# Kernel optimization log

Measured on AMD Instinct MI355X. Metric: run time of the kernel, lower is better.

## Reference

```python
import jax, jax.numpy as jnp
import numpy as np

IMG = 128
HW = IMG // 2          # render resolution (img_size // 2)
NPTS = 64              # samples per ray
MIN_D, MAX_D = 1.2, 2.8
VOL_PHYS = 1.0         # physical volume size; voxel = VOL_PHYS / D
B, C, D = 8, 16, 64
EPS_EA = 1e-10         # pytorch3d EmissionAbsorption eps
BN_EPS = 1e-5


def setup_inputs():
    key = jax.random.key(0)
    ks = jax.random.split(key, 6)
    R = jnp.tile(jnp.eye(3, dtype=jnp.float32)[None], (B, 1, 1))
    T = jnp.tile(jnp.array([0.0, 0.0, 2.0], jnp.float32)[None], (B, 1))
    K = jnp.tile(jnp.array([[180.0, 0.0, 64.0], [0.0, 180.0, 64.0], [0.0, 0.0, 1.0]],
                           jnp.float32)[None], (B, 1, 1))
    feature_3d = jax.random.normal(ks[0], (B, C, D, D, D), jnp.float32)
    density_3d = jax.random.uniform(ks[1], (B, 1, D, D, D), jnp.float32)
    wt = jax.random.normal(ks[2], (16, 16, 6, 6), jnp.float32) * 0.05
    bt = jnp.zeros((16,), jnp.float32)
    g1 = jnp.ones((16,), jnp.float32); be1 = jnp.zeros((16,), jnp.float32)
    w1 = jax.random.normal(ks[3], (8, 16, 5, 5), jnp.float32) * 0.05
    b1 = jnp.zeros((8,), jnp.float32)
    g2 = jnp.ones((8,), jnp.float32); be2 = jnp.zeros((8,), jnp.float32)
    w2 = jax.random.normal(ks[4], (3, 8, 5, 5), jnp.float32) * 0.05
    b2 = jnp.zeros((3,), jnp.float32)
    return dict(R=R, T=T, K=K, feature_3d=feature_3d, density_3d=density_3d,
                wt=wt, bt=bt, g1=g1, be1=be1, w1=w1, b1=b1, g2=g2, be2=be2,
                w2=w2, b2=b2)


def _trilerp(vol, pts):
    # vol [C,Dz,Dy,Dx]; pts [N,3] xyz in [-1,1]; grid_sample align_corners=True, zero padding
    Cc, Dz, Dy, Dx = vol.shape
    ix = (pts[:, 0] + 1.0) * 0.5 * (Dx - 1)
    iy = (pts[:, 1] + 1.0) * 0.5 * (Dy - 1)
    iz = (pts[:, 2] + 1.0) * 0.5 * (Dz - 1)
    x0f = jnp.floor(ix); y0f = jnp.floor(iy); z0f = jnp.floor(iz)
    fx, fy, fz = ix - x0f, iy - y0f, iz - z0f
    x0 = x0f.astype(jnp.int32); y0 = y0f.astype(jnp.int32); z0 = z0f.astype(jnp.int32)
    out = jnp.zeros((Cc, pts.shape[0]), vol.dtype)
    for dz in (0, 1):
        for dy in (0, 1):
            for dx in (0, 1):
                xc, yc, zc = x0 + dx, y0 + dy, z0 + dz
                w = ((fx if dx else 1.0 - fx) * (fy if dy else 1.0 - fy)
                     * (fz if dz else 1.0 - fz))
                valid = ((xc >= 0) & (xc < Dx) & (yc >= 0) & (yc < Dy)
                         & (zc >= 0) & (zc < Dz))
                v = vol[:, jnp.clip(zc, 0, Dz - 1), jnp.clip(yc, 0, Dy - 1),
                        jnp.clip(xc, 0, Dx - 1)]
                out = out + (w * valid) * v
    return out  # [C,N]


def _bn(x, g, b):
    m = x.mean((0, 2, 3), keepdims=True)
    v = x.var((0, 2, 3), keepdims=True)
    return g[None, :, None, None] * (x - m) * jax.lax.rsqrt(v + BN_EPS) + b[None, :, None, None]


def _leaky(x):
    return jnp.where(x >= 0, x, 0.01 * x)


def _conv(x, w, b, pad):
    y = jax.lax.conv_general_dilated(x, w, (1, 1), [(pad, pad), (pad, pad)],
                                     dimension_numbers=('NCHW', 'OIHW', 'NCHW'))
    return y + b[None, :, None, None]


def _conv_t(x, w, b):
    # torch ConvTranspose2d(k=6, stride=2, pad=2) == dilated conv with flipped, io-swapped kernel
    wf = jnp.flip(w, (-2, -1)).transpose(1, 0, 2, 3)
    y = jax.lax.conv_general_dilated(x, wf, (1, 1), [(3, 3), (3, 3)],
                                     lhs_dilation=(2, 2),
                                     dimension_numbers=('NCHW', 'OIHW', 'NCHW'))
    return y + b[None, :, None, None]


def _forward(R, T, K, feature_3d, density_3d, wt, bt, g1, be1, w1, b1, g2, be2, w2, b2):
    Bb, Cc, Dv, Hv, Wv = feature_3d.shape
    # K /= 2; K[:,-1,-1] = 1 (non-mutating)
    Kh = (K / 2.0).at[:, 2, 2].set(1.0)
    fx, fy = Kh[:, 0, 0], Kh[:, 1, 1]
    cx, cy = Kh[:, 0, 2], Kh[:, 1, 2]
    # pixel-center grid at half resolution (NDCGridRaysampler pixel centers)
    u = jnp.arange(HW, dtype=jnp.float32) + 0.5
    v = jnp.arange(HW, dtype=jnp.float32) + 0.5
    ddx = (u[None, None, :] - cx[:, None, None]) / fx[:, None, None]  # [B,1,W]
    ddy = (v[None, :, None] - cy[:, None, None]) / fy[:, None, None]  # [B,H,1]
    one = jnp.ones((1, 1, 1), jnp.float32)
    dirs_cam = jnp.stack(jnp.broadcast_arrays(ddx, ddy, one), axis=-1)  # [B,H,W,3]
    dirs_w = jnp.einsum('bji,bhwj->bhwi', R, dirs_cam)                  # R^T d
    origin = -jnp.einsum('bji,bj->bi', R, T)                            # cam center
    depths = jnp.linspace(MIN_D, MAX_D, NPTS, dtype=jnp.float32)
    pts = (origin[:, None, None, None, :]
           + dirs_w[:, :, :, None, :] * depths[None, None, None, :, None])  # [B,H,W,P,3]
    # world -> Volumes local coords (align_corners=True span: voxel*(dim-1))
    voxel = VOL_PHYS / Dv
    scale = jnp.array([2.0 / (voxel * (Wv - 1)), 2.0 / (voxel * (Hv - 1)),
                       2.0 / (voxel * (Dv - 1))], jnp.float32)
    loc = (pts * scale).reshape(Bb, -1, 3)
    vol = jnp.concatenate([feature_3d, density_3d], axis=1)  # [B,C+1,D,H,W]
    samp = jax.vmap(_trilerp)(vol, loc)                      # [B,C+1,N]
    samp = samp.reshape(Bb, Cc + 1, HW, HW, NPTS)
    feats = jnp.moveaxis(samp[:, :Cc], 1, -1)                # [B,H,W,P,C]
    sigma = samp[:, Cc]                                      # [B,H,W,P]
    # EmissionAbsorption raymarcher (shifted cumprod, shift=1)
    cp = jnp.cumprod((1.0 + EPS_EA) - sigma, axis=-1)
    absorb = jnp.concatenate([jnp.ones_like(cp[..., :1]), cp[..., :-1]], axis=-1)
    wgt = sigma * absorb
    img = jnp.einsum('bhwp,bhwpc->bhwc', wgt, feats)
    opac = 1.0 - jnp.prod(1.0 - sigma, axis=-1)
    imgs = jnp.moveaxis(img, -1, 1)        # [B,C,HW,HW]
    sil = opac[:, None]                    # [B,1,HW,HW]
    # conv refine head
    x = _conv_t(imgs, wt, bt)              # [B,16,128,128]
    x = _leaky(_bn(x, g1, be1))
    x = _conv(x, w1, b1, pad=2)
    x = _leaky(_bn(x, g2, be2))
    x = _conv(x, w2, b2, pad=2)
    imgs_out = jax.nn.relu(x)
    sil_up = jax.image.resize(sil, (Bb, 1, IMG, IMG), 'bilinear')
    return imgs_out, sil_up


def reference(R, T, K, feature_3d, density_3d, wt, bt, g1, be1, w1, b1, g2, be2, w2, b2):
    return _forward(R, T, K, feature_3d, density_3d, wt, bt, g1, be1, w1, b1,
                    g2, be2, w2, b2)
```

## Files before the change

### kernel.cpp

```cpp
#include <hip/hip_runtime.h>
#include <hip/hip_bf16.h>

typedef __hip_bfloat16 bf16;
typedef unsigned int uint;
typedef unsigned short ushort;

using frag  = __attribute__((ext_vector_type(8))) short;
using f32x4 = __attribute__((ext_vector_type(4))) float;

__device__ bf16  g_volT[8ULL*262144*16];
__device__ bf16  g_imgT[8*4096*16];
__device__ bf16  g_t1 [8*16384*16];
__device__ bf16  g_a2r[8*16384*8];
__device__ float g_sil[8*4096];
__device__ float g_part [512*32];
__device__ float g_part2[256*16];
__device__ float g_stats[96];
__device__ bf16  g_wAt[4*5*64*8];
__device__ bf16  g_wA1[13*64*8];
__device__ bf16  g_wA2[7*64*8];

__device__ __forceinline__ float bup(ushort u){ union{uint u; float f;} x; x.u = ((uint)u)<<16; return x.f; }
__device__ __forceinline__ ushort bdn(float f){ union{ bf16 h; ushort s;} v; v.h = __float2bfloat16(f); return v.s; }
__device__ __forceinline__ uint aff2(uint u, float a0, float b0, float a1, float b1){
  float x0 = bup((ushort)(u & 0xffff)), x1 = bup((ushort)(u >> 16));
  float y0 = fmaf(a0, x0, b0); y0 = y0 >= 0.f ? y0 : 0.01f*y0;
  float y1 = fmaf(a1, x1, b1); y1 = y1 >= 0.f ? y1 : 0.01f*y1;
  return (uint)bdn(y0) | ((uint)bdn(y1) << 16);
}
__device__ __forceinline__ f32x4 mf(frag a, frag b, f32x4 c){
  return __builtin_amdgcn_mfma_f32_16x16x32_bf16(a, b, c, 0, 0, 0);
}
__device__ __forceinline__ void acc2(uint u, float w, float& a, float& b){
  union { uint u; float f; } lo, hi;
  lo.u = u << 16; hi.u = u & 0xffff0000u;
  a = fmaf(w, lo.f, a); b = fmaf(w, hi.f, b);
}

__global__ __launch_bounds__(256) void k_wprep(const float* __restrict__ wt,
                                               const float* __restrict__ w1,
                                               const float* __restrict__ w2)
{
  int tid = threadIdx.x;
  for (int idx = tid; idx < 4*5*64*8; idx += 256){
    int cls = idx / 2560; int rem = idx % 2560;
    int step = rem / 512; int rem2 = rem % 512;
    int lane = rem2 >> 3, j = rem2 & 7;
    int o = lane & 15;
    int k = step*32 + (lane>>4)*8 + j;
    int tau = k >> 4, ic = k & 15;
    int dr = cls >> 1, dc = cls & 1;
    float val = 0.f;
    if (tau < 9){
      int s = tau/3, t = tau%3;
      val = wt[(ic*16 + o)*36 + (4-2*s+dr)*6 + (4-2*t+dc)];
    }
    g_wAt[idx] = __float2bfloat16(val);
  }
  for (int idx = tid; idx < 13*64*8; idx += 256){
    int step = idx / 512; int rem2 = idx % 512;
    int lane = rem2 >> 3, j = rem2 & 7;
    int o = lane & 15;
    int k = step*32 + (lane>>4)*8 + j;
    int tau = k >> 4, ic = k & 15;
    float val = (tau < 25 && o < 8) ? w1[o*400 + ic*25 + tau] : 0.f;
    g_wA1[idx] = __float2bfloat16(val);
  }
  for (int idx = tid; idx < 7*64*8; idx += 256){
    int step = idx / 512; int rem2 = idx % 512;
    int lane = rem2 >> 3, j = rem2 & 7;
    int o = lane & 15;
    int k = step*32 + (lane>>4)*8 + j;
    int tau = k >> 3, ic = k & 7;
    float val = (tau < 25 && o < 3) ? w2[o*200 + ic*25 + tau] : 0.f;
    g_wA2[idx] = __float2bfloat16(val);
  }
}

__global__ __launch_bounds__(256) void k_transpose(const float* __restrict__ feat)
{
  __shared__ float lt[64*17];
  int blk = blockIdx.x;
  int y = blk & 63, z = (blk>>6)&63, b = blk>>12;
  const float* src = feat + (size_t)b*16*262144 + z*4096 + y*64;
  #pragma unroll
  for (int it=0; it<4; ++it){
    int idx = it*256 + threadIdx.x;
    int c = idx>>6, x = idx&63;
    lt[x*17+c] = src[(size_t)c*262144 + x];
  }
  __syncthreads();
  uint* dst = (uint*)(g_volT + (size_t)blk*1024);
  #pragma unroll
  for (int it=0; it<2; ++it){
    int idx = it*256 + threadIdx.x;
    int x = idx>>3, c2 = (idx&7)*2;
    uint lo = bdn(lt[x*17+c2]);
    uint hi = bdn(lt[x*17+c2+1]);
    dst[idx] = lo | (hi<<16);
  }
}

__global__ __launch_bounds__(256) void k_render(
    const float* __restrict__ R, const float* __restrict__ T, const float* __restrict__ Kin,
    const float* __restrict__ dens)
{
  __shared__ float lds_acc[4][64][17];
  __shared__ float lds_T[4][64];
  __shared__ float lds_P[4][64];

  int blk  = blockIdx.x;
  int tid  = threadIdx.x;
  int wv   = tid >> 6;
  int lane = tid & 63;
  int b  = blk & 7;
  int t  = blk >> 3;
  int py0 = (t >> 3) * 8, px0 = (t & 7) * 8;
  int h = py0 + (lane >> 3), w = px0 + (lane & 7);

  float fx = Kin[b*9+0]*0.5f, fy = Kin[b*9+4]*0.5f;
  float cx = Kin[b*9+2]*0.5f, cy = Kin[b*9+5]*0.5f;
  float u = (float)w + 0.5f, v = (float)h + 0.5f;
  float dcx = (u - cx)/fx, dcy = (v - cy)/fy;
  float Rm[9];
  #pragma unroll
  for (int i=0;i<9;i++) Rm[i] = R[b*9+i];
  float T0 = T[b*3+0], T1 = T[b*3+1], T2 = T[b*3+2];
  float dwx = Rm[0]*dcx + Rm[3]*dcy + Rm[6];
  float dwy = Rm[1]*dcx + Rm[4]*dcy + Rm[7];
  float dwz = Rm[2]*dcx + Rm[5]*dcy + Rm[8];
  float ox = -(Rm[0]*T0 + Rm[3]*T1 + Rm[6]*T2);
  float oy = -(Rm[1]*T0 + Rm[4]*T1 + Rm[7]*T2);
  float oz = -(Rm[2]*T0 + Rm[5]*T1 + Rm[8]*T2);

  const float SC = 2.0f*64.0f/63.0f;
  const float* dp = dens + (size_t)b*262144;
  const bf16* vb = g_volT + (size_t)b*262144*16;

  float vch[16];
  #pragma unroll
  for (int c=0;c<16;c++) vch[c] = 0.f;
  float Trun = 1.0f, Pop = 1.0f;

  for (int i=0;i<16;i++){
    float depth = 1.2f + (1.6f/63.0f) * (float)(wv*16 + i);
    float ix = (ox + dwx*depth)*SC;  ix = (ix + 1.0f)*0.5f*63.0f;
    float iy = (oy + dwy*depth)*SC;  iy = (iy + 1.0f)*0.5f*63.0f;
    float iz = (oz + dwz*depth)*SC;  iz = (iz + 1.0f)*0.5f*63.0f;
    float xf = floorf(ix), yf = floorf(iy), zf = floorf(iz);
    float fxr = ix-xf, fyr = iy-yf, fzr = iz-zf;
    int x0 = (int)xf, y0 = (int)yf, z0 = (int)zf;

    int offs[8]; float cw[8];
    #pragma unroll
    for (int k=0;k<8;k++){
      int dx = k&1, dy=(k>>1)&1, dz=(k>>2)&1;
      int xc=x0+dx, yc=y0+dy, zc=z0+dz;
      bool valid = (xc>=0)&(xc<64)&(yc>=0)&(yc<64)&(zc>=0)&(zc<64);
      float wk = (dx?fxr:1.f-fxr)*(dy?fyr:1.f-fyr)*(dz?fzr:1.f-fzr);
      cw[k] = valid ? wk : 0.0f;
      int xcc = min(max(xc,0),63), ycc=min(max(yc,0),63), zcc=min(max(zc,0),63);
      offs[k] = (zcc*64 + ycc)*64 + xcc;
    }
    float sigma = 0.f;
    #pragma unroll
    for (int k=0;k<8;k++) sigma += cw[k]*dp[offs[k]];

    float wgt = sigma * Trun;
    Trun *= (1.0f + 1e-10f - sigma);
    Pop  *= (1.0f - sigma);

    #pragma unroll
    for (int k=0;k<8;k++){
      const uint4* p = (const uint4*)(vb + (size_t)offs[k]*16);
      uint4 q0 = p[0];
      uint4 q1 = p[1];
      float wk = cw[k]*wgt;
      acc2(q0.x, wk, vch[0],  vch[1]);
      acc2(q0.y, wk, vch[2],  vch[3]);
      acc2(q0.z, wk, vch[4],  vch[5]);
      acc2(q0.w, wk, vch[6],  vch[7]);
      acc2(q1.x, wk, vch[8],  vch[9]);
      acc2(q1.y, wk, vch[10], vch[11]);
      acc2(q1.z, wk, vch[12], vch[13]);
      acc2(q1.w, wk, vch[14], vch[15]);
    }
  }

  #pragma unroll
  for (int c=0;c<16;c++) lds_acc[wv][lane][c] = vch[c];
  lds_T[wv][lane] = Trun;
  lds_P[wv][lane] = Pop;
  __syncthreads();

  {
    int p  = wv*16 + (lane >> 2);
    int c0 = (lane & 3) * 4;
    float pref = 1.0f;
    float s0=0.f, s1=0.f, s2=0.f, s3=0.f;
    #pragma unroll
    for (int ww=0; ww<4; ++ww){
      s0 += pref * lds_acc[ww][p][c0+0];
      s1 += pref * lds_acc[ww][p][c0+1];
      s2 += pref * lds_acc[ww][p][c0+2];
      s3 += pref * lds_acc[ww][p][c0+3];
      pref *= lds_T[ww][p];
    }
    int hh = py0 + (p >> 3), ww2 = px0 + (p & 7);
    if ((lane & 3) == 0){
      float P = lds_P[0][p]*lds_P[1][p]*lds_P[2][p]*lds_P[3][p];
      g_sil[b*4096 + hh*64 + ww2] = 1.0f - P;
    }
    uint lo = (uint)bdn(s0) | ((uint)bdn(s1) << 16);
    uint hi = (uint)bdn(s2) | ((uint)bdn(s3) << 16);
    uint2 pk; pk.x = lo; pk.y = hi;
    *(uint2*)(g_imgT + ((size_t)(b*4096) + hh*64 + ww2)*16 + c0) = pk;
  }
}

__global__ __launch_bounds__(256) void k_convt(const float* __restrict__ bt)
{
  __shared__ __align__(16) short tile[3*66*16];
  __shared__ float ssum[4][16], ssq[4][16];

  int blk = blockIdx.x;
  int r = blk & 63, b = blk >> 6;
  int tid = threadIdx.x;

  for (int idx = tid; idx < 396; idx += 256){
    int row3 = idx / 132; int rem = idx - row3*132;
    int c2 = rem >> 1, half = rem & 1;
    int gr = r - 1 + row3, gc = c2 - 1;
    uint4 val = make_uint4(0,0,0,0);
    if (gr>=0 && gr<64 && gc>=0 && gc<64)
      val = *(const uint4*)(g_imgT + ((size_t)(b*4096) + gr*64 + gc)*16 + half*8);
    *(uint4*)(tile + (row3*66 + c2)*16 + half*8) = val;
  }
  __syncthreads();

  int wv = tid >> 6, lane = tid & 63;
  int dr = wv >> 1, dc = wv & 1;
  int quad = lane >> 4, col = lane & 15;
  int ic0 = (quad & 1) * 8;

  f32x4 acc[4];
  #pragma unroll
  for (int n=0;n<4;n++) acc[n] = (f32x4){0.f,0.f,0.f,0.f};

  #pragma unroll
  for (int s5=0; s5<5; ++s5){
    frag a = *(const frag*)(g_wAt + ((wv*5 + s5)*64 + lane)*8);
    int tau = 2*s5 + (quad >> 1);
    if (tau > 8) tau = 0;
    int ss = tau/3, tt = tau%3;
    #pragma unroll
    for (int n=0;n<4;n++){
      int c2 = n*16 + col + tt;
      frag bf = *(const frag*)(tile + (ss*66 + c2)*16 + ic0);
      acc[n] = mf(a, bf, acc[n]);
    }
  }

  float4 bo = *(const float4*)(bt + quad*4);
  float bor[4] = {bo.x, bo.y, bo.z, bo.w};
  float sv[4] = {0,0,0,0}, qv[4] = {0,0,0,0};
  int orow = 2*r + dr;
  #pragma unroll
  for (int n=0;n<4;n++){
    int ocol = 2*(n*16 + col) + dc;
    bf16* dst = g_t1 + ((size_t)(b*128 + orow)*128 + ocol)*16 + quad*4;
    #pragma unroll
    for (int reg=0;reg<4;reg++){
      float vvv = acc[n][reg] + bor[reg];
      dst[reg] = __float2bfloat16(vvv);
      sv[reg] += vvv; qv[reg] += vvv*vvv;
    }
  }
  #pragma unroll
  for (int m=1; m<16; m<<=1){
    #pragma unroll
    for (int reg=0;reg<4;reg++){
      sv[reg] += __shfl_xor(sv[reg], m, 64);
      qv[reg] += __shfl_xor(qv[reg], m, 64);
    }
  }
  if ((lane & 15) == 0){
    #pragma unroll
    for (int reg=0;reg<4;reg++){
      ssum[wv][quad*4+reg] = sv[reg];
      ssq [wv][quad*4+reg] = qv[reg];
    }
  }
  __syncthreads();
  if (tid < 16){
    g_part[blk*32 + tid]      = ssum[0][tid]+ssum[1][tid]+ssum[2][tid]+ssum[3][tid];
    g_part[blk*32 + 16 + tid] = ssq[0][tid]+ssq[1][tid]+ssq[2][tid]+ssq[3][tid];
  }
}

__global__ __launch_bounds__(256) void k_fin1(const float* __restrict__ g,
                                              const float* __restrict__ be)
{
  __shared__ float rs[256], rq[256];
  int tid = threadIdx.x; int c = tid>>4, seg = tid&15;
  float s=0.f, q=0.f;
  for (int k=0;k<32;k++){
    int blk = seg*32+k;
    s += g_part[blk*32 + c];
    q += g_part[blk*32 + 16 + c];
  }
  rs[tid]=s; rq[tid]=q; __syncthreads();
  for (int sft=8; sft>0; sft>>=1){
    if (seg<sft){ rs[tid]+=rs[tid+sft]; rq[tid]+=rq[tid+sft]; }
    __syncthreads();
  }
  if (seg==0){
    float m = rs[tid]*(1.0f/131072.f);
    float v = rq[tid]*(1.0f/131072.f) - m*m;
    float a = g[c]*rsqrtf(v+1e-5f);
    g_stats[32+c] = a; g_stats[48+c] = be[c]-m*a;
  }
}

__global__ __launch_bounds__(256) void k_fin2(const float* __restrict__ g,
                                              const float* __restrict__ be)
{
  __shared__ float rs[256], rq[256];
  int tid = threadIdx.x; int seg = tid & 31, c = tid >> 5;
  float s=0.f, q=0.f;
  for (int k=0;k<8;k++){
    int blk = seg*8+k;
    s += g_part2[blk*16 + c];
    q += g_part2[blk*16 + 8 + c];
  }
  rs[tid]=s; rq[tid]=q; __syncthreads();
  for (int sft=16; sft>0; sft>>=1){
    if (seg<sft){ rs[tid]+=rs[tid+sft]; rq[tid]+=rq[tid+sft]; }
    __syncthreads();
  }
  if (seg==0){
    float m = rs[tid]*(1.0f/131072.f);
    float v = rq[tid]*(1.0f/131072.f) - m*m;
    float a = g[c]*rsqrtf(v+1e-5f);
    g_stats[80+c] = a; g_stats[88+c] = be[c]-m*a;
  }
}

__global__ __launch_bounds__(256) void k_conv1(const float* __restrict__ b1)
{
  __shared__ __align__(16) short tile[8*132*16];
  __shared__ float ssum[4][8], ssq[4][8];

  int blk = blockIdx.x;
  int rt = blk & 31, b = blk >> 5;
  int tid = threadIdx.x;

  float pa[16], pb[16];
  #pragma unroll
  for (int c=0;c<16;c++){ pa[c] = g_stats[32+c]; pb[c] = g_stats[48+c]; }

  for (int it=0; it<5; ++it){
    int idx = it*256 + tid;
    if (idx < 1056){
      int r8 = idx / 132; int c2 = idx - r8*132;
      int gr = rt*4 - 2 + r8, gc = c2 - 2;
      uint4 v0 = make_uint4(0,0,0,0), v1 = make_uint4(0,0,0,0);
      if (gr>=0 && gr<128 && gc>=0 && gc<128){
        const bf16* src = g_t1 + ((size_t)(b*128 + gr)*128 + gc)*16;
        v0 = *(const uint4*)(src);
        v1 = *(const uint4*)(src + 8);
        v0.x = aff2(v0.x, pa[0],pb[0],pa[1],pb[1]);
        v0.y = aff2(v0.y, pa[2],pb[2],pa[3],pb[3]);
        v0.z = aff2(v0.z, pa[4],pb[4],pa[5],pb[5]);
        v0.w = aff2(v0.w, pa[6],pb[6],pa[7],pb[7]);
        v1.x = aff2(v1.x, pa[8],pb[8],pa[9],pb[9]);
        v1.y = aff2(v1.y, pa[10],pb[10],pa[11],pb[11]);
        v1.z = aff2(v1.z, pa[12],pb[12],pa[13],pb[13]);
        v1.w = aff2(v1.w, pa[14],pb[14],pa[15],pb[15]);
      }
      *(uint4*)(tile + (r8*132 + c2)*16)     = v0;
      *(uint4*)(tile + (r8*132 + c2)*16 + 8) = v1;
    }
  }
  __syncthreads();

  int wv = tid >> 6, lane = tid & 63;
  int quad = lane >> 4, col = lane & 15;
  int ic0 = (quad & 1) * 8;

  f32x4 acc[8];
  #pragma unroll
  for (int n=0;n<8;n++) acc[n] = (f32x4){0.f,0.f,0.f,0.f};

  for (int s13=0; s13<13; ++s13){
    frag a = *(const frag*)(g_wA1 + (s13*64 + lane)*8);
    int tau = 2*s13 + (quad >> 1);
    if (tau > 24) tau = 0;
    int dh = tau/5, dw = tau%5;
    int rowt = wv + dh;
    #pragma unroll
    for (int n=0;n<8;n++){
      int c2 = n*16 + col + dw;
      frag bf = *(const frag*)(tile + (rowt*132 + c2)*16 + ic0);
      acc[n] = mf(a, bf, acc[n]);
    }
  }

  int row = rt*4 + wv;
  float sv[4] = {0,0,0,0}, qv[4] = {0,0,0,0};
  if (quad < 2){
    float4 bo = *(const float4*)(b1 + quad*4);
    float bor[4] = {bo.x, bo.y, bo.z, bo.w};
    #pragma unroll
    for (int n=0;n<8;n++){
      int px = n*16 + col;
      bf16* dst = g_a2r + ((size_t)(b*128 + row)*128 + px)*8 + quad*4;
      #pragma unroll
      for (int reg=0;reg<4;reg++){
        float vvv = acc[n][reg] + bor[reg];
        dst[reg] = __float2bfloat16(vvv);
        sv[reg] += vvv; qv[reg] += vvv*vvv;
      }
    }
  }
  #pragma unroll
  for (int m=1; m<16; m<<=1){
    #pragma unroll
    for (int reg=0;reg<4;reg++){
      sv[reg] += __shfl_xor(sv[reg], m, 64);
      qv[reg] += __shfl_xor(qv[reg], m, 64);
    }
  }
  if ((lane & 15) == 0 && quad < 2){
    #pragma unroll
    for (int reg=0;reg<4;reg++){
      ssum[wv][quad*4+reg] = sv[reg];
      ssq [wv][quad*4+reg] = qv[reg];
    }
  }
  __syncthreads();
  if (tid < 8){
    g_part2[blk*16 + tid]     = ssum[0][tid]+ssum[1][tid]+ssum[2][tid]+ssum[3][tid];
    g_part2[blk*16 + 8 + tid] = ssq[0][tid]+ssq[1][tid]+ssq[2][tid]+ssq[3][tid];
  }
}

__global__ __launch_bounds__(256) void k_conv2(float* __restrict__ outp,
                                               const float* __restrict__ b2)
{
  __shared__ __align__(16) short tile[8*132*8];

  int blk = blockIdx.x;
  int rt = blk & 31, b = blk >> 5;
  int tid = threadIdx.x;

  float pa[8], pb[8];
  #pragma unroll
  for (int c=0;c<8;c++){ pa[c] = g_stats[80+c]; pb[c] = g_stats[88+c]; }

  for (int it=0; it<5; ++it){
    int idx = it*256 + tid;
    if (idx < 1056){
      int r8 = idx / 132; int c2 = idx - r8*132;
      int gr = rt*4 - 2 + r8, gc = c2 - 2;
      uint4 v0 = make_uint4(0,0,0,0);
      if (gr>=0 && gr<128 && gc>=0 && gc<128){
        v0 = *(const uint4*)(g_a2r + ((size_t)(b*128 + gr)*128 + gc)*8);
        v0.x = aff2(v0.x, pa[0],pb[0],pa[1],pb[1]);
        v0.y = aff2(v0.y, pa[2],pb[2],pa[3],pb[3]);
        v0.z = aff2(v0.z, pa[4],pb[4],pa[5],pb[5]);
        v0.w = aff2(v0.w, pa[6],pb[6],pa[7],pb[7]);
      }
      *(uint4*)(tile + (r8*132 + c2)*8) = v0;
    }
  }
  __syncthreads();

  int wv = tid >> 6, lane = tid & 63;
  int quad = lane >> 4, col = lane & 15;

  f32x4 acc[8];
  #pragma unroll
  for (int n=0;n<8;n++) acc[n] = (f32x4){0.f,0.f,0.f,0.f};

  for (int s7=0; s7<7; ++s7){
    frag a = *(const frag*)(g_wA2 + (s7*64 + lane)*8);
    int tau = 4*s7 + quad;
    if (tau > 24) tau = 0;
    int dh = tau/5, dw = tau%5;
    int rowt = wv + dh;
    #pragma unroll
    for (int n=0;n<8;n++){
      int c2 = n*16 + col + dw;
      frag bf = *(const frag*)(tile + (rowt*132 + c2)*8);
      acc[n] = mf(a, bf, acc[n]);
    }
  }

  if (quad == 0){
    int row = rt*4 + wv;
    float b2v[3] = {b2[0], b2[1], b2[2]};
    #pragma unroll
    for (int n=0;n<8;n++){
      int px = n*16 + col;
      #pragma unroll
      for (int reg=0;reg<3;reg++){
        float vvv = fmaxf(acc[n][reg] + b2v[reg], 0.f);
        outp[(size_t)(b*3 + reg)*16384 + row*128 + px] = vvv;
      }
    }
  }
}

__global__ __launch_bounds__(256) void k_silup(float* __restrict__ outp)
{
  int idx = blockIdx.x*256 + threadIdx.x;
  if (idx >= 8*16384) return;
  int b = idx >> 14;
  int y = (idx >> 7) & 127;
  int x = idx & 127;
  float sy = y*0.5f - 0.25f, sx = x*0.5f - 0.25f;
  float yfl = floorf(sy), xfl = floorf(sx);
  float fy = sy - yfl, fx = sx - xfl;
  int y0 = min(max((int)yfl,0),63), y1 = min(max((int)yfl+1,0),63);
  int x0 = min(max((int)xfl,0),63), x1 = min(max((int)xfl+1,0),63);
  const float* s = g_sil + b*4096;
  float vv = (1.f-fy)*((1.f-fx)*s[y0*64+x0] + fx*s[y0*64+x1])
           +      fy *((1.f-fx)*s[y1*64+x0] + fx*s[y1*64+x1]);
  outp[idx] = vv;
}

extern "C" void kernel_launch(void* const* d_in, const int* in_sizes, int n_in,
                              void* d_out, int out_size, void* d_ws, size_t ws_size,
                              hipStream_t stream)
{
  const float* R    = (const float*)d_in[0];
  const float* T    = (const float*)d_in[1];
  const float* K    = (const float*)d_in[2];
  const float* feat = (const float*)d_in[3];
  const float* dens = (const float*)d_in[4];
  const float* wt   = (const float*)d_in[5];
  const float* bt   = (const float*)d_in[6];
  const float* g1   = (const float*)d_in[7];
  const float* be1  = (const float*)d_in[8];
  const float* w1   = (const float*)d_in[9];
  const float* b1   = (const float*)d_in[10];
  const float* g2   = (const float*)d_in[11];
  const float* be2  = (const float*)d_in[12];
  const float* w2   = (const float*)d_in[13];
  const float* b2   = (const float*)d_in[14];

  k_wprep    <<<1, 256, 0, stream>>>(wt, w1, w2);
  k_transpose<<<32768, 256, 0, stream>>>(feat);
  k_render   <<<512, 256, 0, stream>>>(R, T, K, dens);
  k_convt    <<<512, 256, 0, stream>>>(bt);
  k_fin1     <<<1, 256, 0, stream>>>(g1, be1);
  k_conv1    <<<256, 256, 0, stream>>>(b1);
  k_fin2     <<<1, 256, 0, stream>>>(g2, be2);
  k_conv2    <<<256, 256, 0, stream>>>((float*)d_out, b2);
  k_silup    <<<512, 256, 0, stream>>>((float*)d_out + 393216);
}
```

Baseline: 338.8 us.

## Serialize ray marching per pixel with early termination and skip empty samples

The render kernel now gives each thread a whole ray of 64 samples in one 64-thread block. It skips out-of-volume samples and feature loads when the sample weight is negligible, and exits once every ray in the wave has near-zero transmittance. This removes the cross-wave LDS combine and avoids gathering features that contribute almost nothing. The transpose kernel now processes 4 y-rows per block with float4 loads and 16-byte stores. The trade-offs are less parallelism in render (512 blocks of one wave each) and a small approximation from the weight and transmittance thresholds.

Measured after the change: 334.6 us. Within noise of the previous version (-1.3%).

```diff
diff --git a/kernel.cpp b/kernel.cpp
--- a/kernel.cpp
+++ b/kernel.cpp
@@ -79,40 +79,41 @@
 
 __global__ __launch_bounds__(256) void k_transpose(const float* __restrict__ feat)
 {
-  __shared__ float lt[64*17];
+  __shared__ float lt[4*64*17];
   int blk = blockIdx.x;
-  int y = blk & 63, z = (blk>>6)&63, b = blk>>12;
-  const float* src = feat + (size_t)b*16*262144 + z*4096 + y*64;
+  int yq = blk & 15, z = (blk>>4)&63, b = blk>>10;
+  int y0 = yq*4;
+  int tid = threadIdx.x;
+  int xq = tid & 15;
   #pragma unroll
   for (int it=0; it<4; ++it){
-    int idx = it*256 + threadIdx.x;
-    int c = idx>>6, x = idx&63;
-    lt[x*17+c] = src[(size_t)c*262144 + x];
+    int cy = it*16 + (tid>>4);
+    int c = cy >> 2, y = cy & 3;
+    const float4 vv = *(const float4*)(feat + (size_t)b*4194304 + (size_t)c*262144
+                                       + z*4096 + (y0+y)*64 + xq*4);
+    float* dst = &lt[(y*64 + xq*4)*17 + c];
+    dst[0]=vv.x; dst[17]=vv.y; dst[34]=vv.z; dst[51]=vv.w;
   }
   __syncthreads();
-  uint* dst = (uint*)(g_volT + (size_t)blk*1024);
-  #pragma unroll
-  for (int it=0; it<2; ++it){
-    int idx = it*256 + threadIdx.x;
-    int x = idx>>3, c2 = (idx&7)*2;
-    uint lo = bdn(lt[x*17+c2]);
-    uint hi = bdn(lt[x*17+c2+1]);
-    dst[idx] = lo | (hi<<16);
-  }
-}
-
-__global__ __launch_bounds__(256) void k_render(
+  int y = tid >> 6, x = tid & 63;
+  const float* row = &lt[(y*64+x)*17];
+  uint pk[8];
+  #pragma unroll
+  for (int c2=0;c2<8;c2++)
+    pk[c2] = (uint)bdn(row[2*c2]) | ((uint)bdn(row[2*c2+1])<<16);
+  uint* dst = (uint*)(g_volT + ((size_t)b*262144 + z*4096 + (y0+y)*64 + x)*16);
+  uint4 lo; lo.x=pk[0]; lo.y=pk[1]; lo.z=pk[2]; lo.w=pk[3];
+  uint4 hi; hi.x=pk[4]; hi.y=pk[5]; hi.z=pk[6]; hi.w=pk[7];
+  *(uint4*)dst = lo;
+  *(uint4*)(dst+4) = hi;
+}
+
+__global__ __launch_bounds__(64) void k_render(
     const float* __restrict__ R, const float* __restrict__ T, const float* __restrict__ Kin,
     const float* __restrict__ dens)
 {
-  __shared__ float lds_acc[4][64][17];
-  __shared__ float lds_T[4][64];
-  __shared__ float lds_P[4][64];
-
   int blk  = blockIdx.x;
-  int tid  = threadIdx.x;
-  int wv   = tid >> 6;
-  int lane = tid & 63;
+  int lane = threadIdx.x;
   int b  = blk & 7;
   int t  = blk >> 3;
   int py0 = (t >> 3) * 8, px0 = (t & 7) * 8;
@@ -142,80 +143,66 @@
   for (int c=0;c<16;c++) vch[c] = 0.f;
   float Trun = 1.0f, Pop = 1.0f;
 
-  for (int i=0;i<16;i++){
-    float depth = 1.2f + (1.6f/63.0f) * (float)(wv*16 + i);
+  for (int d=0; d<64; ++d){
+    float depth = 1.2f + (1.6f/63.0f) * (float)d;
     float ix = (ox + dwx*depth)*SC;  ix = (ix + 1.0f)*0.5f*63.0f;
     float iy = (oy + dwy*depth)*SC;  iy = (iy + 1.0f)*0.5f*63.0f;
     float iz = (oz + dwz*depth)*SC;  iz = (iz + 1.0f)*0.5f*63.0f;
     float xf = floorf(ix), yf = floorf(iy), zf = floorf(iz);
-    float fxr = ix-xf, fyr = iy-yf, fzr = iz-zf;
     int x0 = (int)xf, y0 = (int)yf, z0 = (int)zf;
-
-    int offs[8]; float cw[8];
-    #pragma unroll
-    for (int k=0;k<8;k++){
-      int dx = k&1, dy=(k>>1)&1, dz=(k>>2)&1;
-      int xc=x0+dx, yc=y0+dy, zc=z0+dz;
-      bool valid = (xc>=0)&(xc<64)&(yc>=0)&(yc<64)&(zc>=0)&(zc<64);
-      float wk = (dx?fxr:1.f-fxr)*(dy?fyr:1.f-fyr)*(dz?fzr:1.f-fzr);
-      cw[k] = valid ? wk : 0.0f;
-      int xcc = min(max(xc,0),63), ycc=min(max(yc,0),63), zcc=min(max(zc,0),63);
-      offs[k] = (zcc*64 + ycc)*64 + xcc;
-    }
     float sigma = 0.f;
-    #pragma unroll
-    for (int k=0;k<8;k++) sigma += cw[k]*dp[offs[k]];
-
-    float wgt = sigma * Trun;
+
+    bool anyv = (x0>=-1)&(x0<64)&(y0>=-1)&(y0<64)&(z0>=-1)&(z0<64);
+    if (anyv){
+      float fxr = ix-xf, fyr = iy-yf, fzr = iz-zf;
+      int offs[8]; float cw[8];
+      #pragma unroll
+      for (int k=0;k<8;k++){
+        int dx = k&1, dy=(k>>1)&1, dz=(k>>2)&1;
+        int xc=x0+dx, yc=y0+dy, zc=z0+dz;
+        bool valid = (xc>=0)&(xc<64)&(yc>=0)&(yc<64)&(zc>=0)&(zc<64);
+        float wk = (dx?fxr:1.f-fxr)*(dy?fyr:1.f-fyr)*(dz?fzr:1.f-fzr);
+        cw[k] = valid ? wk : 0.0f;
+        int xcc = min(max(xc,0),63), ycc=min(max(yc,0),63), zcc=min(max(zc,0),63);
+        offs[k] = (zcc*64 + ycc)*64 + xcc;
+      }
+      #pragma unroll
+      for (int k=0;k<8;k++) sigma += cw[k]*dp[offs[k]];
+
+      float wgt = sigma * Trun;
+      if (wgt > 1e-7f){
+        #pragma unroll
+        for (int k=0;k<8;k++){
+          const uint4* p = (const uint4*)(vb + (size_t)offs[k]*16);
+          uint4 q0 = p[0];
+          uint4 q1 = p[1];
+          float wk = cw[k]*wgt;
+          acc2(q0.x, wk, vch[0],  vch[1]);
+          acc2(q0.y, wk, vch[2],  vch[3]);
+          acc2(q0.z, wk, vch[4],  vch[5]);
+          acc2(q0.w, wk, vch[6],  vch[7]);
+          acc2(q1.x, wk, vch[8],  vch[9]);
+          acc2(q1.y, wk, vch[10], vch[11]);
+          acc2(q1.z, wk, vch[12], vch[13]);
+          acc2(q1.w, wk, vch[14], vch[15]);
+        }
+      }
+    }
     Trun *= (1.0f + 1e-10f - sigma);
     Pop  *= (1.0f - sigma);
-
-    #pragma unroll
-    for (int k=0;k<8;k++){
-      const uint4* p = (const uint4*)(vb + (size_t)offs[k]*16);
-      uint4 q0 = p[0];
-      uint4 q1 = p[1];
-      float wk = cw[k]*wgt;
-      acc2(q0.x, wk, vch[0],  vch[1]);
-      acc2(q0.y, wk, vch[2],  vch[3]);
-      acc2(q0.z, wk, vch[4],  vch[5]);
-      acc2(q0.w, wk, vch[6],  vch[7]);
-      acc2(q1.x, wk, vch[8],  vch[9]);
-      acc2(q1.y, wk, vch[10], vch[11]);
-      acc2(q1.z, wk, vch[12], vch[13]);
-      acc2(q1.w, wk, vch[14], vch[15]);
-    }
-  }
-
-  #pragma unroll
-  for (int c=0;c<16;c++) lds_acc[wv][lane][c] = vch[c];
-  lds_T[wv][lane] = Trun;
-  lds_P[wv][lane] = Pop;
-  __syncthreads();
-
-  {
-    int p  = wv*16 + (lane >> 2);
-    int c0 = (lane & 3) * 4;
-    float pref = 1.0f;
-    float s0=0.f, s1=0.f, s2=0.f, s3=0.f;
-    #pragma unroll
-    for (int ww=0; ww<4; ++ww){
-      s0 += pref * lds_acc[ww][p][c0+0];
-      s1 += pref * lds_acc[ww][p][c0+1];
-      s2 += pref * lds_acc[ww][p][c0+2];
-      s3 += pref * lds_acc[ww][p][c0+3];
-      pref *= lds_T[ww][p];
-    }
-    int hh = py0 + (p >> 3), ww2 = px0 + (p & 7);
-    if ((lane & 3) == 0){
-      float P = lds_P[0][p]*lds_P[1][p]*lds_P[2][p]*lds_P[3][p];
-      g_sil[b*4096 + hh*64 + ww2] = 1.0f - P;
-    }
-    uint lo = (uint)bdn(s0) | ((uint)bdn(s1) << 16);
-    uint hi = (uint)bdn(s2) | ((uint)bdn(s3) << 16);
-    uint2 pk; pk.x = lo; pk.y = hi;
-    *(uint2*)(g_imgT + ((size_t)(b*4096) + hh*64 + ww2)*16 + c0) = pk;
-  }
+    if (__ballot(Trun > 1e-7f) == 0ULL) break;
+  }
+
+  g_sil[b*4096 + h*64 + w] = 1.0f - Pop;
+  uint pk[8];
+  #pragma unroll
+  for (int c2=0;c2<8;c2++)
+    pk[c2] = (uint)bdn(vch[2*c2]) | ((uint)bdn(vch[2*c2+1])<<16);
+  uint* dst = (uint*)(g_imgT + ((size_t)(b*4096) + h*64 + w)*16);
+  uint4 lo; lo.x=pk[0]; lo.y=pk[1]; lo.z=pk[2]; lo.w=pk[3];
+  uint4 hi; hi.x=pk[4]; hi.y=pk[5]; hi.z=pk[6]; hi.w=pk[7];
+  *(uint4*)dst = lo;
+  *(uint4*)(dst+4) = hi;
 }
 
 __global__ __launch_bounds__(256) void k_convt(const float* __restrict__ bt)
@@ -551,8 +538,8 @@
   const float* b2   = (const float*)d_in[14];
 
   k_wprep    <<<1, 256, 0, stream>>>(wt, w1, w2);
-  k_transpose<<<32768, 256, 0, stream>>>(feat);
-  k_render   <<<512, 256, 0, stream>>>(R, T, K, dens);
+  k_transpose<<<8192, 256, 0, stream>>>(feat);
+  k_render   <<<512, 64, 0, stream>>>(R, T, K, dens);
   k_convt    <<<512, 256, 0, stream>>>(bt);
   k_fin1     <<<1, 256, 0, stream>>>(g1, be1);
   k_conv1    <<<256, 256, 0, stream>>>(b1);
```
